# Kernel optimization log

Measured on AMD Instinct MI355X. Metric: run time of the kernel, lower is better.

## Reference

```python
import jax, jax.numpy as jnp
import numpy as np

IN_MODES = (8, 8, 8, 8)
OUT_MODES = (8, 8, 8, 8)
R = 16
RANKS = (1, R, R, R, 1)
BATCH = 8192
PROD_IN = int(np.prod(IN_MODES))   # 4096
PROD_OUT = int(np.prod(OUT_MODES))  # 4096


def setup_inputs() -> dict:
    key = jax.random.key(0)
    ks = jax.random.split(key, 6)
    # matches reset_normal() init scale
    CONST = ((0.05 ** 2 / np.prod(RANKS)) ** (1.0 / (len(RANKS) - 1))) ** 0.5
    P0 = jax.random.normal(ks[0], (OUT_MODES[0] * IN_MODES[0], R, 1), jnp.float32) * CONST
    P1 = jax.random.normal(ks[1], (OUT_MODES[1] * IN_MODES[1], R, R), jnp.float32) * CONST
    P2 = jax.random.normal(ks[2], (OUT_MODES[2] * IN_MODES[2], R, R), jnp.float32) * CONST
    P3 = jax.random.normal(ks[3], (OUT_MODES[3] * IN_MODES[3], R, 1), jnp.float32) * CONST
    bias = jnp.zeros((PROD_OUT,), jnp.float32)
    x = jax.random.normal(ks[5], (BATCH, PROD_IN), jnp.float32)
    return {"x": x, "P0": P0, "P1": P1, "P2": P2, "P3": P3, "bias": bias}


def _cayley(P):
    # Batched Cayley transform: Q = (I - A) @ inv(I + A), A skew from triu(P,1).
    # P: (n, r, r)
    T = jnp.triu(P, 1)
    A = T - jnp.swapaxes(T, -1, -2)
    I = jnp.eye(P.shape[-1], dtype=P.dtype)
    return jnp.einsum('nij,njk->nik', I - A, jnp.linalg.inv(I + A))


def _core(Q, o, m, r_in, r_out, first):
    # Q: (o*m, r, c) stacked in (j, k) order -> U: (r, o, m, c) as in getU
    r, c = Q.shape[1], Q.shape[2]
    U = Q.reshape(o, m, r, c).transpose(2, 0, 1, 3)  # (r, o, m, c)
    if first:
        U = jnp.swapaxes(U, 0, 3)  # (c=1, o, m, r)
    return U.reshape(o * r_out, m * r_in)  # G_i: (o_i * ranks[i+1], m_i * ranks[i])


def _build_cores(P0, P1, P2, P3):
    G0 = _core(P0, OUT_MODES[0], IN_MODES[0], RANKS[0], RANKS[1], True)
    G1 = _core(_cayley(P1), OUT_MODES[1], IN_MODES[1], RANKS[1], RANKS[2], False)
    G2 = _core(_cayley(P2), OUT_MODES[2], IN_MODES[2], RANKS[2], RANKS[3], False)
    G3 = _core(P3, OUT_MODES[3], IN_MODES[3], RANKS[3], RANKS[4], False)
    return [G0, G1, G2, G3]


def _tt_dot(x, G, bias):
    res = x.reshape(-1, PROD_IN).T  # (prod_in, B)
    for ii in range(4):
        res = res.reshape(RANKS[ii] * IN_MODES[ii], -1)
        res = G[ii] @ res                       # (o_i * r_{i+1}, rest)
        res = res.reshape(OUT_MODES[ii], -1).T  # rotate processed mode to back
    res = res.reshape(-1, PROD_OUT)
    return res + bias


def reference(x, P0, P1, P2, P3, bias):
    G = _build_cores(P0, P1, P2, P3)
    return _tt_dot(x, G, bias)
```

## Files before the change

### kernel.cpp

```cpp
#include <hip/hip_runtime.h>
#include <hip/hip_bf16.h>

typedef __attribute__((ext_vector_type(8))) short sh8;
typedef __attribute__((ext_vector_type(16))) float fx16;
typedef __attribute__((ext_vector_type(4))) unsigned int u32x4;

__device__ __forceinline__ unsigned short f2bits(float a) {
  union { __hip_bfloat16 h; unsigned short u; } c;
  c.h = __float2bfloat16(a);
  return c.u;
}
__device__ __forceinline__ unsigned int pkcvt(float a, float b) {
  unsigned int r;
  asm("v_cvt_pk_bf16_f32 %0, %1, %2" : "=v"(r) : "v"(a), "v"(b));
  return r;
}
__device__ __forceinline__ fx16 fzero16() {
  fx16 z;
  #pragma unroll
  for (int i = 0; i < 16; ++i) z[i] = 0.0f;
  return z;
}

__global__ void k_cayley(const float* __restrict__ P1, const float* __restrict__ P2,
                         float* __restrict__ Qout) {
  int t = blockIdx.x * blockDim.x + threadIdx.x;
  int mat = t >> 4;
  int row = t & 15;
  if (mat >= 128) return;
  const float* P = (mat < 64) ? (P1 + mat * 256) : (P2 + (mat - 64) * 256);
  float M[16], Rr[16];
  #pragma unroll
  for (int j = 0; j < 16; ++j) {
    float a = 0.0f;
    if (j > row) a = P[row * 16 + j];
    if (j < row) a = -P[j * 16 + row];
    float d = (j == row) ? 1.0f : 0.0f;
    M[j]  = d + a;
    Rr[j] = d - a;
  }
  int gbase = (threadIdx.x & 63) & ~15;
  #pragma unroll
  for (int k = 0; k < 16; ++k) {
    float pkk = __shfl(M[k], gbase + k);
    float inv = 1.0f / pkk;
    float pM[16], pR[16];
    #pragma unroll
    for (int j = 0; j < 16; ++j) {
      pM[j] = __shfl(M[j], gbase + k) * inv;
      pR[j] = __shfl(Rr[j], gbase + k) * inv;
    }
    if (row == k) {
      #pragma unroll
      for (int j = 0; j < 16; ++j) { M[j] = pM[j]; Rr[j] = pR[j]; }
    } else {
      float f = M[k];
      #pragma unroll
      for (int j = 0; j < 16; ++j) { M[j] -= f * pM[j]; Rr[j] -= f * pR[j]; }
    }
  }
  float* qo = Qout + mat * 256 + row * 16;
  #pragma unroll
  for (int j = 0; j < 16; ++j) qo[j] = Rr[j];
}

__global__ void k_build(const float* __restrict__ P0, const float* __restrict__ P3,
                        const float* __restrict__ Qbuf,
                        unsigned short* __restrict__ W1, unsigned short* __restrict__ W2) {
  int t = blockIdx.x * blockDim.x + threadIdx.x;
  if (t >= 131072) return;
  const float* Q1 = Qbuf;
  const float* Q2 = Qbuf + 16384;
  int e  = t & 65535;
  int r  = e & 7;
  int l  = (e >> 3) & 63;
  int kx = (e >> 9) & 3;
  int mt = (e >> 11) & 1;
  int t2 = (e >> 12) & 15;
  float acc = 0.0f;
  if (t < 65536) {
    int m = mt * 32 + (l & 31);
    int q = kx * 16 + ((l >> 5) << 3) + r;
    int j0 = m >> 3, j1 = m & 7, i0 = q >> 3, i1 = q & 7;
    #pragma unroll
    for (int t1 = 0; t1 < 16; ++t1) {
      float c0 = P0[(j0 * 8 + (t1 >> 1)) * 16 + ((t1 & 1) * 8 + i0)];
      int a1 = j1 * 16 + t2, u1 = t1 * 8 + i1;
      float c1 = Q1[((a1 & 7) * 8 + (u1 >> 4)) * 256 + (a1 >> 3) * 16 + (u1 & 15)];
      acc += c0 * c1;
    }
    W1[e] = f2bits(acc);
  } else {
    int n = mt * 32 + (l & 31);
    int s = kx * 16 + (r & 3) + 8 * (r >> 2) + 4 * (l >> 5);
    int j2 = n >> 3, j3 = n & 7, i2 = s >> 3, i3 = s & 7;
    #pragma unroll
    for (int t3 = 0; t3 < 16; ++t3) {
      int a2 = j2 * 16 + t3, u2 = t2 * 8 + i2;
      float c2 = Q2[((a2 & 7) * 8 + (u2 >> 4)) * 256 + (a2 >> 3) * 16 + (u2 & 15)];
      float c3 = P3[((t3 & 7) * 8 + i3) * 16 + (j3 * 2 + (t3 >> 3))];
      acc += c2 * c3;
    }
    W2[e] = f2bits(acc);
  }
}

__global__ __launch_bounds__(256, 2) void k_main(
    const float* __restrict__ x,
    const unsigned short* __restrict__ W1,
    const unsigned short* __restrict__ W2,
    const float* __restrict__ bias,
    float* __restrict__ out) {
  __shared__ __align__(16) char XsT[4 * 8192];

  const int tid  = threadIdx.x;
  const int lane = tid & 63;
  const int w    = tid >> 6;
  const int h    = lane >> 5;
  const int l31  = lane & 31;
  const int ep   = (w >> 1) * 2;
  const int mh   = w & 1;
  const size_t bbase = (size_t)blockIdx.x * 4;

  {
    const int s = lane;
    const float* xb = x + (bbase + w) * 4096;
    const unsigned sw = ((unsigned)(s & 7)) << 4;
    char* base = XsT + w * 8192 + s * 128;
    #pragma unroll
    for (int c = 0; c < 4; ++c) {
      unsigned int d[8];
      #pragma unroll
      for (int jj = 0; jj < 8; ++jj) {
        float a  = xb[(c * 16 + 2 * jj + 0) * 64 + s];
        float bq = xb[(c * 16 + 2 * jj + 1) * 64 + s];
        d[jj] = pkcvt(a, bq);
      }
      u32x4 v0 = {d[0], d[1], d[2], d[3]};
      u32x4 v1 = {d[4], d[5], d[6], d[7]};
      *(u32x4*)(base + (((unsigned)(c * 32)) ^ sw))      = v0;
      *(u32x4*)(base + (((unsigned)(c * 32 + 16)) ^ sw)) = v1;
    }
  }
  __syncthreads();

  sh8 af[2][2][4];
  #pragma unroll
  for (int e = 0; e < 2; ++e) {
    const char* myX = XsT + (ep + e) * 8192;
    #pragma unroll
    for (int st = 0; st < 2; ++st)
      #pragma unroll
      for (int kq = 0; kq < 4; ++kq) {
        int srow = st * 32 + l31;
        unsigned boff = (unsigned)srow * 128 +
                        (((unsigned)(kq * 32 + h * 16)) ^ (((unsigned)(srow & 7)) << 4));
        af[e][st][kq] = *(const sh8*)(myX + boff);
      }
  }

  const fx16 zc = fzero16();
  fx16 accO[2][2];
  accO[0][0] = zc; accO[0][1] = zc;
  accO[1][0] = zc; accO[1][1] = zc;

  const sh8* w1f = (const sh8*)W1;
  const sh8* w2f = (const sh8*)W2;

  sh8 b1[4];
  #pragma unroll
  for (int kq = 0; kq < 4; ++kq)
    b1[kq] = w1f[(mh * 4 + kq) * 64 + lane];

  #pragma unroll 1
  for (int t2 = 0; t2 < 16; ++t2) {
    sh8 b2[2][4];
    #pragma unroll
    for (int nt = 0; nt < 2; ++nt)
      #pragma unroll
      for (int ks = 0; ks < 4; ++ks)
        b2[nt][ks] = w2f[t2 * 512 + (nt * 4 + ks) * 64 + lane];

    fx16 accY[2];
    __builtin_amdgcn_s_setprio(1);
    accY[0] = __builtin_amdgcn_mfma_f32_32x32x16_bf16(af[0][0][0], b1[0], zc, 0, 0, 0);
    accY[1] = __builtin_amdgcn_mfma_f32_32x32x16_bf16(af[0][1][0], b1[0], zc, 0, 0, 0);
    #pragma unroll
    for (int kq = 1; kq < 4; ++kq) {
      accY[0] = __builtin_amdgcn_mfma_f32_32x32x16_bf16(af[0][0][kq], b1[kq], accY[0], 0, 0, 0);
      accY[1] = __builtin_amdgcn_mfma_f32_32x32x16_bf16(af[0][1][kq], b1[kq], accY[1], 0, 0, 0);
    }
    __builtin_amdgcn_s_setprio(0);

    sh8 ga0[4];
    #pragma unroll
    for (int st = 0; st < 2; ++st) {
      fx16 Y = accY[st];
      union { u32x4 u; sh8 s8; } c0, c1;
      c0.u = (u32x4){pkcvt(Y[0], Y[1]),  pkcvt(Y[2], Y[3]),
                     pkcvt(Y[4], Y[5]),  pkcvt(Y[6], Y[7])};
      c1.u = (u32x4){pkcvt(Y[8], Y[9]),  pkcvt(Y[10], Y[11]),
                     pkcvt(Y[12], Y[13]), pkcvt(Y[14], Y[15])};
      ga0[st * 2 + 0] = c0.s8;
      ga0[st * 2 + 1] = c1.s8;
    }

    fx16 accZ[2];
    __builtin_amdgcn_s_setprio(1);
    accZ[0] = __builtin_amdgcn_mfma_f32_32x32x16_bf16(af[1][0][0], b1[0], zc, 0, 0, 0);
    accZ[1] = __builtin_amdgcn_mfma_f32_32x32x16_bf16(af[1][1][0], b1[0], zc, 0, 0, 0);
    #pragma unroll
    for (int kq = 1; kq < 4; ++kq) {
      accZ[0] = __builtin_amdgcn_mfma_f32_32x32x16_bf16(af[1][0][kq], b1[kq], accZ[0], 0, 0, 0);
      accZ[1] = __builtin_amdgcn_mfma_f32_32x32x16_bf16(af[1][1][kq], b1[kq], accZ[1], 0, 0, 0);
    }
    __builtin_amdgcn_s_setprio(0);

    {
      const int t2n = (t2 + 1) & 15;
      #pragma unroll
      for (int kq = 0; kq < 4; ++kq)
        b1[kq] = w1f[t2n * 512 + (mh * 4 + kq) * 64 + lane];
    }

    __builtin_amdgcn_s_setprio(1);
    #pragma unroll
    for (int ks = 0; ks < 4; ++ks) {
      accO[0][0] = __builtin_amdgcn_mfma_f32_32x32x16_bf16(ga0[ks], b2[0][ks], accO[0][0], 0, 0, 0);
      accO[0][1] = __builtin_amdgcn_mfma_f32_32x32x16_bf16(ga0[ks], b2[1][ks], accO[0][1], 0, 0, 0);
    }
    __builtin_amdgcn_s_setprio(0);

    sh8 ga1[4];
    #pragma unroll
    for (int st = 0; st < 2; ++st) {
      fx16 Y = accZ[st];
      union { u32x4 u; sh8 s8; } c0, c1;
      c0.u = (u32x4){pkcvt(Y[0], Y[1]),  pkcvt(Y[2], Y[3]),
                     pkcvt(Y[4], Y[5]),  pkcvt(Y[6], Y[7])};
      c1.u = (u32x4){pkcvt(Y[8], Y[9]),  pkcvt(Y[10], Y[11]),
                     pkcvt(Y[12], Y[13]), pkcvt(Y[14], Y[15])};
      ga1[st * 2 + 0] = c0.s8;
      ga1[st * 2 + 1] = c1.s8;
    }

    __builtin_amdgcn_s_setprio(1);
    #pragma unroll
    for (int ks = 0; ks < 4; ++ks) {
      accO[1][0] = __builtin_amdgcn_mfma_f32_32x32x16_bf16(ga1[ks], b2[0][ks], accO[1][0], 0, 0, 0);
      accO[1][1] = __builtin_amdgcn_mfma_f32_32x32x16_bf16(ga1[ks], b2[1][ks], accO[1][1], 0, 0, 0);
    }
    __builtin_amdgcn_s_setprio(0);
  }

  #pragma unroll
  for (int e = 0; e < 2; ++e) {
    float* ob = out + (bbase + ep + e) * 4096;
    #pragma unroll
    for (int nt = 0; nt < 2; ++nt) {
      #pragma unroll
      for (int reg = 0; reg < 16; ++reg) {
        int m = mh * 32 + (reg & 3) + 8 * (reg >> 2) + 4 * h;
        int n = nt * 32 + l31;
        int o = m * 64 + n;
        ob[o] = accO[e][nt][reg] + bias[o];
      }
    }
  }
}

extern "C" void kernel_launch(void* const* d_in, const int* in_sizes, int n_in,
                              void* d_out, int out_size, void* d_ws, size_t ws_size,
                              hipStream_t stream) {
  (void)n_in; (void)out_size; (void)ws_size;
  const float* x    = (const float*)d_in[0];
  const float* P0   = (const float*)d_in[1];
  const float* P1   = (const float*)d_in[2];
  const float* P2   = (const float*)d_in[3];
  const float* P3   = (const float*)d_in[4];
  const float* bias = (const float*)d_in[5];
  float* out = (float*)d_out;

  float* Qbuf = (float*)d_ws;
  unsigned short* W1 = (unsigned short*)((char*)d_ws + 131072);
  unsigned short* W2 = (unsigned short*)((char*)d_ws + 262144);

  k_cayley<<<8, 256, 0, stream>>>(P1, P2, Qbuf);
  k_build<<<512, 256, 0, stream>>>(P0, P3, Qbuf, W1, W2);

  int batch = in_sizes[0] / 4096;
  k_main<<<batch / 4, 256, 0, stream>>>(x, W1, W2, bias, out);
}
```

Baseline: 144.6 us.

## Stage W1/W2 weight tiles through double-buffered LDS with direct global-to-LDS loads

Each iteration's W1 and W2 tiles are now copied into a double-buffered shared-memory area with global_load_lds, prefetching the next tile while the current one is computed. Fragments are read from LDS instead of straight from global memory, so the four waves share one copy of the weights per block and cut redundant global/L2 traffic. The cost is an extra 32 KB of LDS per block, which may limit occupancy, plus a vmcnt wait and block barrier on every iteration.

Measured after the change: 139.0 us. 3.9% less time.

```diff
diff --git a/kernel.cpp b/kernel.cpp
--- a/kernel.cpp
+++ b/kernel.cpp
@@ -111,7 +111,9 @@
     const unsigned short* __restrict__ W2,
     const float* __restrict__ bias,
     float* __restrict__ out) {
-  __shared__ __align__(16) char XsT[4 * 8192];
+  __shared__ __align__(16) char smem[4 * 8192 + 2 * 16384];
+  char* XsT = smem;
+  char* WL  = smem + 32768;
 
   const int tid  = threadIdx.x;
   const int lane = tid & 63;
@@ -121,6 +123,21 @@
   const int ep   = (w >> 1) * 2;
   const int mh   = w & 1;
   const size_t bbase = (size_t)blockIdx.x * 4;
+
+  const char* w1c = (const char*)W1;
+  const char* w2c = (const char*)W2;
+
+  {
+    char* dst = WL;
+    #pragma unroll
+    for (int c = 0; c < 4; ++c) {
+      const char* src = (c < 2) ? (w1c + c * 4096) : (w2c + (c - 2) * 4096);
+      src += w * 1024 + lane * 16;
+      __builtin_amdgcn_global_load_lds((const unsigned int*)src,
+                                       (unsigned int*)(dst + c * 4096 + w * 1024),
+                                       16, 0, 0);
+    }
+  }
 
   {
     const int s = lane;
@@ -142,6 +159,7 @@
       *(u32x4*)(base + (((unsigned)(c * 32 + 16)) ^ sw)) = v1;
     }
   }
+  asm volatile("s_waitcnt vmcnt(0)" ::: "memory");
   __syncthreads();
 
   sh8 af[2][2][4];
@@ -164,22 +182,34 @@
   accO[0][0] = zc; accO[0][1] = zc;
   accO[1][0] = zc; accO[1][1] = zc;
 
-  const sh8* w1f = (const sh8*)W1;
-  const sh8* w2f = (const sh8*)W2;
-
-  sh8 b1[4];
-  #pragma unroll
-  for (int kq = 0; kq < 4; ++kq)
-    b1[kq] = w1f[(mh * 4 + kq) * 64 + lane];
-
   #pragma unroll 1
   for (int t2 = 0; t2 < 16; ++t2) {
+    char* cur = WL + (t2 & 1) * 16384;
+
+    if (t2 < 15) {
+      char* dst = WL + ((t2 + 1) & 1) * 16384;
+      const size_t toff = (size_t)(t2 + 1) * 8192;
+      #pragma unroll
+      for (int c = 0; c < 4; ++c) {
+        const char* src = (c < 2) ? (w1c + toff + c * 4096)
+                                  : (w2c + toff + (c - 2) * 4096);
+        src += w * 1024 + lane * 16;
+        __builtin_amdgcn_global_load_lds((const unsigned int*)src,
+                                         (unsigned int*)(dst + c * 4096 + w * 1024),
+                                         16, 0, 0);
+      }
+    }
+
+    sh8 b1[4];
+    #pragma unroll
+    for (int kq = 0; kq < 4; ++kq)
+      b1[kq] = *(const sh8*)(cur + (((mh * 4 + kq) * 64 + lane) << 4));
     sh8 b2[2][4];
     #pragma unroll
     for (int nt = 0; nt < 2; ++nt)
       #pragma unroll
       for (int ks = 0; ks < 4; ++ks)
-        b2[nt][ks] = w2f[t2 * 512 + (nt * 4 + ks) * 64 + lane];
+        b2[nt][ks] = *(const sh8*)(cur + 8192 + (((nt * 4 + ks) * 64 + lane) << 4));
 
     fx16 accY[2];
     __builtin_amdgcn_s_setprio(1);
@@ -214,16 +244,7 @@
       accZ[0] = __builtin_amdgcn_mfma_f32_32x32x16_bf16(af[1][0][kq], b1[kq], accZ[0], 0, 0, 0);
       accZ[1] = __builtin_amdgcn_mfma_f32_32x32x16_bf16(af[1][1][kq], b1[kq], accZ[1], 0, 0, 0);
     }
-    __builtin_amdgcn_s_setprio(0);
-
-    {
-      const int t2n = (t2 + 1) & 15;
-      #pragma unroll
-      for (int kq = 0; kq < 4; ++kq)
-        b1[kq] = w1f[t2n * 512 + (mh * 4 + kq) * 64 + lane];
-    }
-
-    __builtin_amdgcn_s_setprio(1);
+
     #pragma unroll
     for (int ks = 0; ks < 4; ++ks) {
       accO[0][0] = __builtin_amdgcn_mfma_f32_32x32x16_bf16(ga0[ks], b2[0][ks], accO[0][0], 0, 0, 0);
@@ -251,6 +272,9 @@
       accO[1][1] = __builtin_amdgcn_mfma_f32_32x32x16_bf16(ga1[ks], b2[1][ks], accO[1][1], 0, 0, 0);
     }
     __builtin_amdgcn_s_setprio(0);
+
+    asm volatile("s_waitcnt vmcnt(0)" ::: "memory");
+    __syncthreads();
   }
 
   #pragma unroll
```

## Stage W2 tiles through LDS with double-buffered async global-to-LDS loads

Applied to the files above, without the earlier changes.

Each block now loads the W2 weight tiles into LDS with global_load_lds and double-buffers them, prefetching tile t2+1 while tile t2 is consumed, instead of every wave reading W2 fragments from global memory into registers each iteration. The goal is to take the global-load latency off the MFMA loop and to share one copy of W2 across the four waves. In exchange it adds 16 KB of LDS, one barrier and a vmcnt(0) wait per iteration, and a reordering of where the b2 fragments get loaded. The extra LDS and the per-iteration sync may reduce occupancy or cause stalls.

Result: faster. 138.0 us (-4.6%).

```diff
diff --git a/kernel.cpp b/kernel.cpp
--- a/kernel.cpp
+++ b/kernel.cpp
@@ -111,7 +111,9 @@
     const unsigned short* __restrict__ W2,
     const float* __restrict__ bias,
     float* __restrict__ out) {
-  __shared__ __align__(16) char XsT[4 * 8192];
+  __shared__ __align__(16) char smem[4 * 8192 + 2 * 8192];
+  char* XsT = smem;
+  char* WL  = smem + 32768;
 
   const int tid  = threadIdx.x;
   const int lane = tid & 63;
@@ -121,6 +123,22 @@
   const int ep   = (w >> 1) * 2;
   const int mh   = w & 1;
   const size_t bbase = (size_t)blockIdx.x * 4;
+
+  const char* w2c = (const char*)W2;
+  const sh8* w1f = (const sh8*)W1;
+
+  #pragma unroll
+  for (int c = 0; c < 2; ++c) {
+    const char* src = w2c + c * 4096 + w * 1024 + lane * 16;
+    __builtin_amdgcn_global_load_lds((const unsigned int*)src,
+                                     (unsigned int*)(WL + c * 4096 + w * 1024),
+                                     16, 0, 0);
+  }
+
+  sh8 b1[4];
+  #pragma unroll
+  for (int kq = 0; kq < 4; ++kq)
+    b1[kq] = w1f[(mh * 4 + kq) * 64 + lane];
 
   {
     const int s = lane;
@@ -142,6 +160,7 @@
       *(u32x4*)(base + (((unsigned)(c * 32 + 16)) ^ sw)) = v1;
     }
   }
+  asm volatile("s_waitcnt vmcnt(0)" ::: "memory");
   __syncthreads();
 
   sh8 af[2][2][4];
@@ -164,22 +183,26 @@
   accO[0][0] = zc; accO[0][1] = zc;
   accO[1][0] = zc; accO[1][1] = zc;
 
-  const sh8* w1f = (const sh8*)W1;
-  const sh8* w2f = (const sh8*)W2;
-
-  sh8 b1[4];
-  #pragma unroll
-  for (int kq = 0; kq < 4; ++kq)
-    b1[kq] = w1f[(mh * 4 + kq) * 64 + lane];
-
   #pragma unroll 1
   for (int t2 = 0; t2 < 16; ++t2) {
-    sh8 b2[2][4];
-    #pragma unroll
-    for (int nt = 0; nt < 2; ++nt)
-      #pragma unroll
-      for (int ks = 0; ks < 4; ++ks)
-        b2[nt][ks] = w2f[t2 * 512 + (nt * 4 + ks) * 64 + lane];
+    char* cur = WL + (t2 & 1) * 8192;
+
+    if (t2 < 15) {
+      char* dst = WL + ((t2 + 1) & 1) * 8192;
+      const size_t toff = (size_t)(t2 + 1) * 8192;
+      #pragma unroll
+      for (int c = 0; c < 2; ++c) {
+        const char* src = w2c + toff + c * 4096 + w * 1024 + lane * 16;
+        __builtin_amdgcn_global_load_lds((const unsigned int*)src,
+                                         (unsigned int*)(dst + c * 4096 + w * 1024),
+                                         16, 0, 0);
+      }
+    }
+
+    sh8 b2a[4];
+    #pragma unroll
+    for (int ks = 0; ks < 4; ++ks)
+      b2a[ks] = *(const sh8*)(cur + (((0 * 4 + ks) * 64 + lane) << 4));
 
     fx16 accY[2];
     __builtin_amdgcn_s_setprio(1);
@@ -205,6 +228,11 @@
       ga0[st * 2 + 1] = c1.s8;
     }
 
+    sh8 b2b[4];
+    #pragma unroll
+    for (int ks = 0; ks < 4; ++ks)
+      b2b[ks] = *(const sh8*)(cur + (((1 * 4 + ks) * 64 + lane) << 4));
+
     fx16 accZ[2];
     __builtin_amdgcn_s_setprio(1);
     accZ[0] = __builtin_amdgcn_mfma_f32_32x32x16_bf16(af[1][0][0], b1[0], zc, 0, 0, 0);
@@ -226,8 +254,8 @@
     __builtin_amdgcn_s_setprio(1);
     #pragma unroll
     for (int ks = 0; ks < 4; ++ks) {
-      accO[0][0] = __builtin_amdgcn_mfma_f32_32x32x16_bf16(ga0[ks], b2[0][ks], accO[0][0], 0, 0, 0);
-      accO[0][1] = __builtin_amdgcn_mfma_f32_32x32x16_bf16(ga0[ks], b2[1][ks], accO[0][1], 0, 0, 0);
+      accO[0][0] = __builtin_amdgcn_mfma_f32_32x32x16_bf16(ga0[ks], b2a[ks], accO[0][0], 0, 0, 0);
+      accO[0][1] = __builtin_amdgcn_mfma_f32_32x32x16_bf16(ga0[ks], b2b[ks], accO[0][1], 0, 0, 0);
     }
     __builtin_amdgcn_s_setprio(0);
 
@@ -247,10 +275,13 @@
     __builtin_amdgcn_s_setprio(1);
     #pragma unroll
     for (int ks = 0; ks < 4; ++ks) {
-      accO[1][0] = __builtin_amdgcn_mfma_f32_32x32x16_bf16(ga1[ks], b2[0][ks], accO[1][0], 0, 0, 0);
-      accO[1][1] = __builtin_amdgcn_mfma_f32_32x32x16_bf16(ga1[ks], b2[1][ks], accO[1][1], 0, 0, 0);
+      accO[1][0] = __builtin_amdgcn_mfma_f32_32x32x16_bf16(ga1[ks], b2a[ks], accO[1][0], 0, 0, 0);
+      accO[1][1] = __builtin_amdgcn_mfma_f32_32x32x16_bf16(ga1[ks], b2b[ks], accO[1][1], 0, 0, 0);
     }
     __builtin_amdgcn_s_setprio(0);
+
+    asm volatile("s_waitcnt vmcnt(0)" ::: "memory");
+    __syncthreads();
   }
 
   #pragma unroll
```
